# Performance work log

Hardware: AMD Instinct MI355X
Metric: run time of the kernel (lower is better)

The kernel has to match this reference:

```python
import jax, jax.numpy as jnp
import numpy as np

N, E, IN_C, HID_C, OUT_C = 50000, 800000, 64, 64, 8
NEG_SLOPE = 0.2


def setup_inputs() -> dict:
    key = jax.random.key(0)
    ks = jax.random.split(key, 12)
    return {
        "x": jax.random.normal(ks[0], (N, IN_C), dtype=jnp.float32),
        "edge_index": jax.random.randint(ks[1], (2, E), 0, N, dtype=jnp.int64),
        "edge_value": jax.random.uniform(ks[2], (E,), dtype=jnp.float32),
        "W1": jax.random.normal(ks[3], (IN_C, HID_C), dtype=jnp.float32) * 0.1,
        "a1_src": jax.random.normal(ks[4], (HID_C,), dtype=jnp.float32) * 0.1,
        "a1_dst": jax.random.normal(ks[5], (HID_C,), dtype=jnp.float32) * 0.1,
        "b1": jnp.zeros((HID_C,), dtype=jnp.float32),
        "W2": jax.random.normal(ks[6], (HID_C, OUT_C), dtype=jnp.float32) * 0.1,
        "a2_src": jax.random.normal(ks[7], (OUT_C,), dtype=jnp.float32) * 0.1,
        "a2_dst": jax.random.normal(ks[8], (OUT_C,), dtype=jnp.float32) * 0.1,
        "b2": jnp.zeros((OUT_C,), dtype=jnp.float32),
    }


def _rgat_conv(x, src, dst, edge_value, W, a_src, a_dst, b, n_nodes):
    # Linear transform: [N, out_c]
    h = x @ W
    # Per-node attention halves, gathered per edge -> per-edge logit
    e_src = h @ a_src  # [N]
    e_dst = h @ a_dst  # [N]
    logits = jax.nn.leaky_relu(e_src[src] + e_dst[dst], negative_slope=NEG_SLOPE)  # [E]
    # Segment softmax over destination neighborhoods (numerically stable)
    m = jax.ops.segment_max(logits, dst, num_segments=n_nodes)  # [N]
    ex = jnp.exp(logits - m[dst])
    denom = jax.ops.segment_sum(ex, dst, num_segments=n_nodes)  # [N]
    alpha = ex / (denom[dst] + 1e-16)  # [E]
    # Edge-weighted messages, scatter-aggregate to destinations
    msg = (alpha * edge_value)[:, None] * h[src]  # [E, out_c]
    out = jax.ops.segment_sum(msg, dst, num_segments=n_nodes)  # [N, out_c]
    return out + b


def reference(x, edge_index, edge_value, W1, a1_src, a1_dst, b1, W2, a2_src, a2_dst, b2):
    src, dst = edge_index[0], edge_index[1]
    n = x.shape[0]
    hid = _rgat_conv(x, src, dst, edge_value, W1, a1_src, a1_dst, b1, n)
    hid = jax.nn.relu(hid)
    out = _rgat_conv(hid, src, dst, edge_value, W2, a2_src, a2_dst, b2, n)
    return jax.nn.log_softmax(out, axis=1)
```

## Files before the change

### kernel.cpp

```cpp
#include <hip/hip_runtime.h>
#include <hip/hip_fp16.h>
#include <math.h>


#define CHUNK 4096
#define NBKT  256
#define CAP   6144
#define NPW   4

typedef unsigned long long ull;
typedef float v2f __attribute__((ext_vector_type(2)));

struct PartSmem {
    int lhist[NBKT], lbase[NBKT], lcur[NBKT], gbase[NBKT];
    ull buf[CHUNK];
};
struct GemmSmem {
    float4 Wl[64 * 16];
    float  Xt[64 * 64];
};
union FusedSmem { PartSmem p; GemmSmem g; };


__global__ void __launch_bounds__(256) part_gemm_kernel(
    const int* __restrict__ src, const int* __restrict__ dst,
    const float* __restrict__ ev, int* __restrict__ bcnt,
    ull* __restrict__ ped, int E, int nchunks,
    const float* __restrict__ x, const float* __restrict__ W,
    const float* __restrict__ a_src, const float* __restrict__ a_dst,
    unsigned* __restrict__ h, float* __restrict__ es, float* __restrict__ ed,
    int N)
{
    __shared__ FusedSmem sm;
    const int t = threadIdx.x;

    if (blockIdx.x < nchunks) {
        int e0 = blockIdx.x * CHUNK;
        int cnt = min(CHUNK, E - e0);
        sm.p.lhist[t] = 0;
        __syncthreads();
        for (int i = t; i < cnt; i += 256)
            atomicAdd(&sm.p.lhist[dst[e0 + i] >> 8], 1);
        __syncthreads();
        int myc = sm.p.lhist[t];
        sm.p.lbase[t] = myc;
        __syncthreads();
        for (int o = 1; o < 256; o <<= 1) {
            int add = (t >= o) ? sm.p.lbase[t - o] : 0;
            __syncthreads();
            sm.p.lbase[t] += add;
            __syncthreads();
        }
        int excl = sm.p.lbase[t] - myc;
        sm.p.gbase[t] = myc ? atomicAdd(&bcnt[t], myc) : 0;
        __syncthreads();
        sm.p.lbase[t] = excl;
        sm.p.lcur[t] = excl;
        __syncthreads();
        for (int i = t; i < cnt; i += 256) {
            int e = e0 + i;
            int d = dst[e];
            int b = d >> 8;
            unsigned p = (unsigned)src[e] | ((unsigned)(d & 255) << 16)
                       | ((unsigned)b << 24);
            ull q = (ull)p | ((ull)__float_as_uint(ev[e]) << 32);
            int r = atomicAdd(&sm.p.lcur[b], 1);
            sm.p.buf[r] = q;
        }
        __syncthreads();
        for (int i = t; i < cnt; i += 256) {
            ull q = sm.p.buf[i];
            int b = (int)((q >> 24) & 255);
            ped[(size_t)b * CAP + sm.p.gbase[b] + i - sm.p.lbase[b]] = q;
        }
        return;
    }

    const int n0 = (blockIdx.x - nchunks) * 64;

    #pragma unroll
    for (int i = 0; i < 4; ++i)
        sm.g.Wl[t + i * 256] = ((const float4*)W)[t + i * 256];

    #pragma unroll
    for (int i = 0; i < 4; ++i) {
        int f   = t + i * 256;
        int row = f >> 4, kq = f & 15;
        int grow = n0 + row;
        float4 v = make_float4(0.f, 0.f, 0.f, 0.f);
        if (grow < N) v = ((const float4*)x)[(size_t)grow * 16 + kq];
        int rs = row ^ ((kq & 3) << 2);
        sm.g.Xt[(kq * 4 + 0) * 64 + rs] = v.x;
        sm.g.Xt[(kq * 4 + 1) * 64 + rs] = v.y;
        sm.g.Xt[(kq * 4 + 2) * 64 + rs] = v.z;
        sm.g.Xt[(kq * 4 + 3) * 64 + rs] = v.w;
    }

    const int tx = t & 15;
    const int ty = t >> 4;
    const float4 asv = ((const float4*)a_src)[tx];
    const float4 adv = ((const float4*)a_dst)[tx];
    __syncthreads();

    float4 acc0 = make_float4(0.f,0.f,0.f,0.f);
    float4 acc1 = make_float4(0.f,0.f,0.f,0.f);
    float4 acc2 = make_float4(0.f,0.f,0.f,0.f);
    float4 acc3 = make_float4(0.f,0.f,0.f,0.f);

    #pragma unroll 8
    for (int k = 0; k < 64; ++k) {
        int swz = (k >> 2) & 3;
        const float4 xr = *(const float4*)&sm.g.Xt[k * 64 + ((ty ^ swz) << 2)];
        const float4 wv = sm.g.Wl[k * 16 + tx];
        acc0.x += xr.x * wv.x; acc0.y += xr.x * wv.y;
        acc0.z += xr.x * wv.z; acc0.w += xr.x * wv.w;
        acc1.x += xr.y * wv.x; acc1.y += xr.y * wv.y;
        acc1.z += xr.y * wv.z; acc1.w += xr.y * wv.w;
        acc2.x += xr.z * wv.x; acc2.y += xr.z * wv.y;
        acc2.z += xr.z * wv.z; acc2.w += xr.z * wv.w;
        acc3.x += xr.w * wv.x; acc3.y += xr.w * wv.y;
        acc3.z += xr.w * wv.z; acc3.w += xr.w * wv.w;
    }

    float4 accs[4] = {acc0, acc1, acc2, acc3};
    #pragma unroll
    for (int r = 0; r < 4; ++r) {
        int grow = n0 + ty * 4 + r;
        float4 a = accs[r];
        if (grow < N) {
            int lo = __builtin_amdgcn_cvt_pk_fp8_f32(a.x, a.y, 0, false);
            int pk = __builtin_amdgcn_cvt_pk_fp8_f32(a.z, a.w, lo, true);
            h[(size_t)grow * 16 + tx] = (unsigned)pk;
        }
        float ps = a.x * asv.x + a.y * asv.y + a.z * asv.z + a.w * asv.w;
        float pd = a.x * adv.x + a.y * adv.y + a.z * adv.z + a.w * adv.w;
        #pragma unroll
        for (int o = 8; o > 0; o >>= 1) {
            ps += __shfl_xor(ps, o);
            pd += __shfl_xor(pd, o);
        }
        if (tx == 0 && grow < N) { es[grow] = ps; ed[grow] = pd; }
    }
}


__global__ void __launch_bounds__(1024) csr2_kernel(
    const ull* __restrict__ ped, const int* __restrict__ bcnt,
    int* __restrict__ off, int* __restrict__ deg,
    ull* __restrict__ csre, int N)
{
    __shared__ int cl[256], sc[256], cur[256];
    int b = blockIdx.x, t = threadIdx.x;
    const int cnt = min(bcnt[b], CAP);
    const size_t base = (size_t)b * CAP;
    if (t < 256) cl[t] = 0;
    __syncthreads();
    for (int i = t; i < cnt; i += 1024)
        atomicAdd(&cl[(int)((ped[base + i] >> 16) & 255)], 1);
    __syncthreads();
    int myc = (t < 256) ? cl[t] : 0;
    if (t < 256) sc[t] = myc;
    __syncthreads();
    for (int o = 1; o < 256; o <<= 1) {
        int add = (t >= o && t < 256) ? sc[t - o] : 0;
        __syncthreads();
        if (t < 256) sc[t] += add;
        __syncthreads();
    }
    if (t < 256) {
        int excl = sc[t] - myc;
        int node = b * 256 + t;
        if (node < N) { off[node] = (int)base + excl; deg[node] = myc; }
        cur[t] = excl;
    }
    __syncthreads();
    for (int i = t; i < cnt; i += 1024) {
        ull q = ped[base + i];
        int dloc = (int)((q >> 16) & 255);
        int pos = (int)base + atomicAdd(&cur[dloc], 1);
        csre[pos] = (q & 0xFFFFFFFF00000000ull) | (q & 0xFFFFull);
    }
}


__global__ void __launch_bounds__(256) agg64_fused_kernel(
    const int* __restrict__ off, const int* __restrict__ deg,
    const ull* __restrict__ csre,
    const float* __restrict__ es, const float* __restrict__ ed,
    const unsigned* __restrict__ h, const float* __restrict__ b1,
    const float* __restrict__ W2, const float* __restrict__ a2s,
    const float* __restrict__ a2d, float* __restrict__ h2,
    float* __restrict__ es2, float* __restrict__ ed2, int N)
{
    const int wid = threadIdx.x >> 6, lane = threadIdx.x & 63;
    const int g  = lane >> 4;
    const int c4 = lane & 15;
    const int n0 = (blockIdx.x * 4 + wid) * NPW;
    if (n0 >= N) return;
    const int n1 = min(n0 + NPW, N);

    const int c0 = 2 * g, c1 = 2 * g + 1;
    float w2r0[4], w2r1[4];
    #pragma unroll
    for (int j = 0; j < 4; ++j) {
        w2r0[j] = W2[(4 * c4 + j) * 8 + c0];
        w2r1[j] = W2[(4 * c4 + j) * 8 + c1];
    }
    const float4 b1v = *(const float4*)&b1[c4 << 2];
    const float a2sv0 = a2s[c0], a2sv1 = a2s[c1];
    const float a2dv0 = a2d[c0], a2dv1 = a2d[c1];

    int offv = 0, degv = 0;
    float edv = 0.f;
    {
        int nn = n0 + (lane & (NPW - 1));
        if (nn < N) { offv = off[nn]; degv = deg[nn]; edv = ed[nn]; }
    }

    int svS; float evS, esS;
    unsigned pu0, pu1, pu2, pu3;
    {
        int begX = __shfl(offv, 0);
        int cntX = min(__shfl(degv, 0), 64);
        int idxX = begX + min(lane, max(cntX, 1) - 1);
        ull recX = csre[idxX];
        svS = (int)(recX & 0xFFFFull);
        evS = __uint_as_float((unsigned)(recX >> 32));
        esS = es[svS];
        int s0 = __shfl(svS, g),     s1 = __shfl(svS, 4 + g);
        int s2 = __shfl(svS, 8 + g), s3 = __shfl(svS, 12 + g);
        pu0 = h[(size_t)s0 * 16 + c4];
        pu1 = h[(size_t)s1 * 16 + c4];
        pu2 = h[(size_t)s2 * 16 + c4];
        pu3 = h[(size_t)s3 * 16 + c4];
    }

    for (int n = n0; n < n1; ++n) {
        const int nl = n - n0;
        const int beg = __shfl(offv, nl);
        const int dg  = __shfl(degv, nl);
        const float edn = __shfl(edv, nl);
        const int cnt0 = min(dg, 64);

        const int   sv = svS;
        float z = esS + edn;
        float l = z > 0.f ? z : 0.2f * z;
        float q = (lane < cnt0) ? __expf(l) : 0.f;
        float den = q;
        const float wv = q * evS;

        const unsigned cu0 = pu0, cu1 = pu1, cu2 = pu2, cu3 = pu3;

        if (n + 1 < n1) {
            int begX = __shfl(offv, nl + 1);
            int cntX = min(__shfl(degv, nl + 1), 64);
            int idxX = begX + min(lane, max(cntX, 1) - 1);
            ull recX = csre[idxX];
            svS = (int)(recX & 0xFFFFull);
            evS = __uint_as_float((unsigned)(recX >> 32));
            esS = es[svS];
            int s0 = __shfl(svS, g),     s1 = __shfl(svS, 4 + g);
            int s2 = __shfl(svS, 8 + g), s3 = __shfl(svS, 12 + g);
            pu0 = h[(size_t)s0 * 16 + c4];
            pu1 = h[(size_t)s1 * 16 + c4];
            pu2 = h[(size_t)s2 * 16 + c4];
            pu3 = h[(size_t)s3 * 16 + c4];
        }

        float4 acc = make_float4(0.f, 0.f, 0.f, 0.f);
        {
            float w0 = __shfl(wv, g),     w1 = __shfl(wv, 4 + g);
            float w2 = __shfl(wv, 8 + g), w3 = __shfl(wv, 12 + g);
            v2f f0a = __builtin_amdgcn_cvt_pk_f32_fp8((int)cu0, false);
            v2f f0b = __builtin_amdgcn_cvt_pk_f32_fp8((int)cu0, true);
            v2f f1a = __builtin_amdgcn_cvt_pk_f32_fp8((int)cu1, false);
            v2f f1b = __builtin_amdgcn_cvt_pk_f32_fp8((int)cu1, true);
            v2f f2a = __builtin_amdgcn_cvt_pk_f32_fp8((int)cu2, false);
            v2f f2b = __builtin_amdgcn_cvt_pk_f32_fp8((int)cu2, true);
            v2f f3a = __builtin_amdgcn_cvt_pk_f32_fp8((int)cu3, false);
            v2f f3b = __builtin_amdgcn_cvt_pk_f32_fp8((int)cu3, true);
            acc.x += w0 * f0a.x + w1 * f1a.x + w2 * f2a.x + w3 * f3a.x;
            acc.y += w0 * f0a.y + w1 * f1a.y + w2 * f2a.y + w3 * f3a.y;
            acc.z += w0 * f0b.x + w1 * f1b.x + w2 * f2b.x + w3 * f3b.x;
            acc.w += w0 * f0b.y + w1 * f1b.y + w2 * f2b.y + w3 * f3b.y;
        }
        for (int j = 16; j < cnt0; j += 16) {
            int j0 = j + g, j1 = j + 4 + g, j2 = j + 8 + g, j3 = j + 12 + g;
            int   s0 = __shfl(sv, j0), s1 = __shfl(sv, j1);
            int   s2 = __shfl(sv, j2), s3 = __shfl(sv, j3);
            float w0 = __shfl(wv, j0), w1 = __shfl(wv, j1);
            float w2 = __shfl(wv, j2), w3 = __shfl(wv, j3);
            const unsigned u0 = h[(size_t)s0 * 16 + c4];
            const unsigned u1 = h[(size_t)s1 * 16 + c4];
            const unsigned u2 = h[(size_t)s2 * 16 + c4];
            const unsigned u3 = h[(size_t)s3 * 16 + c4];
            v2f f0a = __builtin_amdgcn_cvt_pk_f32_fp8((int)u0, false);
            v2f f0b = __builtin_amdgcn_cvt_pk_f32_fp8((int)u0, true);
            v2f f1a = __builtin_amdgcn_cvt_pk_f32_fp8((int)u1, false);
            v2f f1b = __builtin_amdgcn_cvt_pk_f32_fp8((int)u1, true);
            v2f f2a = __builtin_amdgcn_cvt_pk_f32_fp8((int)u2, false);
            v2f f2b = __builtin_amdgcn_cvt_pk_f32_fp8((int)u2, true);
            v2f f3a = __builtin_amdgcn_cvt_pk_f32_fp8((int)u3, false);
            v2f f3b = __builtin_amdgcn_cvt_pk_f32_fp8((int)u3, true);
            acc.x += w0 * f0a.x + w1 * f1a.x + w2 * f2a.x + w3 * f3a.x;
            acc.y += w0 * f0a.y + w1 * f1a.y + w2 * f2a.y + w3 * f3a.y;
            acc.z += w0 * f0b.x + w1 * f1b.x + w2 * f2b.x + w3 * f3b.x;
            acc.w += w0 * f0b.y + w1 * f1b.y + w2 * f2b.y + w3 * f3b.y;
        }
        for (int base = beg + 64; base < beg + dg; base += 64) {
            const int cnt = min(beg + dg - base, 64);
            const int idx = base + min(lane, cnt - 1);
            const ull rec = csre[idx];
            const int sv2 = (int)(rec & 0xFFFFull);
            const float ev2 = __uint_as_float((unsigned)(rec >> 32));
            float z2 = es[sv2] + edn;
            float l2 = z2 > 0.f ? z2 : 0.2f * z2;
            float q2 = (lane < cnt) ? __expf(l2) : 0.f;
            den += q2;
            const float wv2 = q2 * ev2;
            for (int j = 0; j < cnt; j += 16) {
                int j0 = j + g, j1 = j + 4 + g, j2 = j + 8 + g, j3 = j + 12 + g;
                int   s0 = __shfl(sv2, j0), s1 = __shfl(sv2, j1);
                int   s2 = __shfl(sv2, j2), s3 = __shfl(sv2, j3);
                float w0 = __shfl(wv2, j0), w1 = __shfl(wv2, j1);
                float w2 = __shfl(wv2, j2), w3 = __shfl(wv2, j3);
                const unsigned u0 = h[(size_t)s0 * 16 + c4];
                const unsigned u1 = h[(size_t)s1 * 16 + c4];
                const unsigned u2 = h[(size_t)s2 * 16 + c4];
                const unsigned u3 = h[(size_t)s3 * 16 + c4];
                v2f f0a = __builtin_amdgcn_cvt_pk_f32_fp8((int)u0, false);
                v2f f0b = __builtin_amdgcn_cvt_pk_f32_fp8((int)u0, true);
                v2f f1a = __builtin_amdgcn_cvt_pk_f32_fp8((int)u1, false);
                v2f f1b = __builtin_amdgcn_cvt_pk_f32_fp8((int)u1, true);
                v2f f2a = __builtin_amdgcn_cvt_pk_f32_fp8((int)u2, false);
                v2f f2b = __builtin_amdgcn_cvt_pk_f32_fp8((int)u2, true);
                v2f f3a = __builtin_amdgcn_cvt_pk_f32_fp8((int)u3, false);
                v2f f3b = __builtin_amdgcn_cvt_pk_f32_fp8((int)u3, true);
                acc.x += w0 * f0a.x + w1 * f1a.x + w2 * f2a.x + w3 * f3a.x;
                acc.y += w0 * f0a.y + w1 * f1a.y + w2 * f2a.y + w3 * f3a.y;
                acc.z += w0 * f0b.x + w1 * f1b.x + w2 * f2b.x + w3 * f3b.x;
                acc.w += w0 * f0b.y + w1 * f1b.y + w2 * f2b.y + w3 * f3b.y;
            }
        }

        #pragma unroll
        for (int o = 16; o < 64; o <<= 1) {
            acc.x += __shfl_xor(acc.x, o);
            acc.y += __shfl_xor(acc.y, o);
            acc.z += __shfl_xor(acc.z, o);
            acc.w += __shfl_xor(acc.w, o);
        }
        #pragma unroll
        for (int o = 1; o < 64; o <<= 1) den += __shfl_xor(den, o);

        const float inv = 1.f / (den + 1e-16f);
        float4 hid;
        hid.x = fmaxf(acc.x * inv + b1v.x, 0.f);
        hid.y = fmaxf(acc.y * inv + b1v.y, 0.f);
        hid.z = fmaxf(acc.z * inv + b1v.z, 0.f);
        hid.w = fmaxf(acc.w * inv + b1v.w, 0.f);

        float p0 = hid.x * w2r0[0] + hid.y * w2r0[1] + hid.z * w2r0[2] + hid.w * w2r0[3];
        float p1 = hid.x * w2r1[0] + hid.y * w2r1[1] + hid.z * w2r1[2] + hid.w * w2r1[3];
        #pragma unroll
        for (int o = 1; o < 16; o <<= 1) {
            p0 += __shfl_xor(p0, o);
            p1 += __shfl_xor(p1, o);
        }
        float psv = p0 * a2sv0 + p1 * a2sv1;
        float pdv = p0 * a2dv0 + p1 * a2dv1;
        #pragma unroll
        for (int o = 16; o < 64; o <<= 1) {
            psv += __shfl_xor(psv, o);
            pdv += __shfl_xor(pdv, o);
        }
        if (c4 == 0)
            *(float2*)&h2[(size_t)n * 8 + c0] = make_float2(p0, p1);
        if (lane == 0) { es2[n] = psv; ed2[n] = pdv; }
    }
}


__global__ void __launch_bounds__(256) agg8_lsm_kernel(
    const int* __restrict__ off, const int* __restrict__ deg,
    const ull* __restrict__ csre,
    const float* __restrict__ es, const float* __restrict__ ed,
    const float* __restrict__ h2, const float* __restrict__ b,
    float* __restrict__ out, int N)
{
    const int wid = threadIdx.x >> 6, lane = threadIdx.x & 63;
    const int g  = lane >> 2;
    const int cp = lane & 3;
    const int n0 = (blockIdx.x * 4 + wid) * NPW;
    if (n0 >= N) return;
    const int n1 = min(n0 + NPW, N);
    const float bc0 = b[2 * cp], bc1 = b[2 * cp + 1];

    int offv = 0, degv = 0;
    float edv = 0.f;
    {
        int nn = n0 + (lane & (NPW - 1));
        if (nn < N) { offv = off[nn]; degv = deg[nn]; edv = ed[nn]; }
    }

    int svS; float evS, esS;
    float2 pf0, pf1;
    {
        int begX = __shfl(offv, 0);
        int cntX = min(__shfl(degv, 0), 64);
        int idxX = begX + min(lane, max(cntX, 1) - 1);
        ull recX = csre[idxX];
        svS = (int)(recX & 0xFFFFull);
        evS = __uint_as_float((unsigned)(recX >> 32));
        esS = es[svS];
        int s0 = __shfl(svS, g), s1 = __shfl(svS, 16 + g);
        pf0 = *(const float2*)&h2[(size_t)s0 * 8 + 2 * cp];
        pf1 = *(const float2*)&h2[(size_t)s1 * 8 + 2 * cp];
    }

    for (int n = n0; n < n1; ++n) {
        const int nl = n - n0;
        const int beg = __shfl(offv, nl);
        const int dg  = __shfl(degv, nl);
        const float edn = __shfl(edv, nl);
        const int cnt0 = min(dg, 64);

        const int   sv = svS;
        float z = esS + edn;
        float l = z > 0.f ? z : 0.2f * z;
        float q = (lane < cnt0) ? __expf(l) : 0.f;
        float den = q;
        const float wv = q * evS;

        const float2 cf0 = pf0, cf1 = pf1;

        if (n + 1 < n1) {
            int begX = __shfl(offv, nl + 1);
            int cntX = min(__shfl(degv, nl + 1), 64);
            int idxX = begX + min(lane, max(cntX, 1) - 1);
            ull recX = csre[idxX];
            svS = (int)(recX & 0xFFFFull);
            evS = __uint_as_float((unsigned)(recX >> 32));
            esS = es[svS];
            int s0 = __shfl(svS, g), s1 = __shfl(svS, 16 + g);
            pf0 = *(const float2*)&h2[(size_t)s0 * 8 + 2 * cp];
            pf1 = *(const float2*)&h2[(size_t)s1 * 8 + 2 * cp];
        }

        float a0, a1;
        {
            float w0 = __shfl(wv, g), w1 = __shfl(wv, 16 + g);
            a0 = w0 * cf0.x + w1 * cf1.x;
            a1 = w0 * cf0.y + w1 * cf1.y;
        }
        for (int j = 32; j < cnt0; j += 32) {
            int j0 = j + g, j1 = j + 16 + g;
            int   s0 = __shfl(sv, j0), s1 = __shfl(sv, j1);
            float w0 = __shfl(wv, j0), w1 = __shfl(wv, j1);
            const float2 f0 = *(const float2*)&h2[(size_t)s0 * 8 + 2 * cp];
            const float2 f1 = *(const float2*)&h2[(size_t)s1 * 8 + 2 * cp];
            a0 += w0 * f0.x + w1 * f1.x;
            a1 += w0 * f0.y + w1 * f1.y;
        }
        for (int base = beg + 64; base < beg + dg; base += 64) {
            const int cnt = min(beg + dg - base, 64);
            const int idx = base + min(lane, cnt - 1);
            const ull rec = csre[idx];
            const int sv2 = (int)(rec & 0xFFFFull);
            const float ev2 = __uint_as_float((unsigned)(rec >> 32));
            float z2 = es[sv2] + edn;
            float l2 = z2 > 0.f ? z2 : 0.2f * z2;
            float q2 = (lane < cnt) ? __expf(l2) : 0.f;
            den += q2;
            const float wv2 = q2 * ev2;
            for (int j = 0; j < cnt; j += 32) {
                int j0 = j + g, j1 = j + 16 + g;
                int   s0 = __shfl(sv2, j0), s1 = __shfl(sv2, j1);
                float w0 = __shfl(wv2, j0), w1 = __shfl(wv2, j1);
                const float2 f0 = *(const float2*)&h2[(size_t)s0 * 8 + 2 * cp];
                const float2 f1 = *(const float2*)&h2[(size_t)s1 * 8 + 2 * cp];
                a0 += w0 * f0.x + w1 * f1.x;
                a1 += w0 * f0.y + w1 * f1.y;
            }
        }

        #pragma unroll
        for (int o = 4; o < 64; o <<= 1) {
            a0 += __shfl_xor(a0, o);
            a1 += __shfl_xor(a1, o);
        }
        #pragma unroll
        for (int o = 1; o < 64; o <<= 1) den += __shfl_xor(den, o);

        const float inv = 1.f / (den + 1e-16f);
        float v0 = a0 * inv + bc0;
        float v1 = a1 * inv + bc1;
        float vm = fmaxf(v0, v1);
        vm = fmaxf(vm, __shfl_xor(vm, 1));
        vm = fmaxf(vm, __shfl_xor(vm, 2));
        float s = __expf(v0 - vm) + __expf(v1 - vm);
        s += __shfl_xor(s, 1);
        s += __shfl_xor(s, 2);
        float lse = vm + logf(s);
        if (lane < 4)
            *(float2*)&out[(size_t)n * 8 + 2 * cp] = make_float2(v0 - lse, v1 - lse);
    }
}


extern "C" void kernel_launch(void* const* d_in, const int* in_sizes, int n_in,
                              void* d_out, int out_size, void* d_ws, size_t ws_size,
                              hipStream_t stream)
{
    const float* x   = (const float*)d_in[0];
    const int*   ei  = (const int*)d_in[1];
    const float* ev  = (const float*)d_in[2];
    const float* W1  = (const float*)d_in[3];
    const float* a1s = (const float*)d_in[4];
    const float* a1d = (const float*)d_in[5];
    const float* b1  = (const float*)d_in[6];
    const float* W2  = (const float*)d_in[7];
    const float* a2s = (const float*)d_in[8];
    const float* a2d = (const float*)d_in[9];
    const float* b2  = (const float*)d_in[10];
    float* out = (float*)d_out;

    const int N = in_sizes[0] / 64;
    const int E = in_sizes[2];
    const int* srcp = ei;
    const int* dstp = ei + E;
    const int nchunks = (E + CHUNK - 1) / CHUNK;
    const int ngemm   = (N + 63) / 64;
    const int nbuck = (N + 255) / 256;
    const int nodes_per_block = 4 * NPW;

    ull*   ped  = (ull*)d_ws;
    ull*   csre = ped + (size_t)NBKT * CAP;
    int*   bcnt = (int*)(csre + (size_t)NBKT * CAP);
    int*   off  = bcnt + NBKT;
    int*   deg  = off + N;
    float* es1  = (float*)(deg + N);
    float* ed1  = es1 + N;
    float* es2  = ed1 + N;
    float* ed2  = es2 + N;
    unsigned* h1 = (unsigned*)(ed2 + N);
    float* h2   = (float*)(h1 + (size_t)N * 16);

    hipMemsetAsync(bcnt, 0, NBKT * sizeof(int), stream);

    part_gemm_kernel<<<nchunks + ngemm, 256, 0, stream>>>(
        srcp, dstp, ev, bcnt, ped, E, nchunks,
        x, W1, a1s, a1d, h1, es1, ed1, N);

    csr2_kernel<<<nbuck, 1024, 0, stream>>>(ped, bcnt, off, deg, csre, N);

    agg64_fused_kernel<<<(N + nodes_per_block - 1) / nodes_per_block, 256, 0, stream>>>(
        off, deg, csre, es1, ed1, h1, b1, W2, a2s, a2d, h2, es2, ed2, N);

    agg8_lsm_kernel<<<(N + nodes_per_block - 1) / nodes_per_block, 256, 0, stream>>>(
        off, deg, csre, es2, ed2, h2, b2, out, N);
}
```

Measured before the change: 158.2 us.

## Precompute layer-1 attention weights and denominators during CSR build

Moves the layer-1 edge logit, exp, edge-value product and softmax denominator into the CSR construction kernel. Per-destination sums are accumulated with shared-memory atomics, and each CSR record now stores the final weight, so the layer-1 aggregation kernel no longer gathers es or computes exp or a wavefront reduction. Because the stored weight replaces the raw edge value, the CSR kernel also writes separate source-index and edge-value arrays for a new layer-2 kernel. That adds extra global writes and workspace, and the old agg8 kernel is left as a stub full of casts to void.

Measured after the change: 167.5 us. 1.06x slower.

```diff
diff --git a/kernel.cpp b/kernel.cpp
--- a/kernel.cpp
+++ b/kernel.cpp
@@ -146,14 +146,21 @@
 
 __global__ void __launch_bounds__(1024) csr2_kernel(
     const ull* __restrict__ ped, const int* __restrict__ bcnt,
-    int* __restrict__ off, int* __restrict__ deg,
+    const float* __restrict__ es1, const float* __restrict__ ed1,
+    int* __restrict__ off, int* __restrict__ deg, float* __restrict__ den1,
     ull* __restrict__ csre, int N)
 {
     __shared__ int cl[256], sc[256], cur[256];
+    __shared__ float edl[256], denl[256];
     int b = blockIdx.x, t = threadIdx.x;
     const int cnt = min(bcnt[b], CAP);
     const size_t base = (size_t)b * CAP;
-    if (t < 256) cl[t] = 0;
+    if (t < 256) {
+        cl[t] = 0;
+        denl[t] = 0.f;
+        int node = b * 256 + t;
+        edl[t] = (node < N) ? ed1[node] : 0.f;
+    }
     __syncthreads();
     for (int i = t; i < cnt; i += 1024)
         atomicAdd(&cl[(int)((ped[base + i] >> 16) & 255)], 1);
@@ -175,18 +182,29 @@
     }
     __syncthreads();
     for (int i = t; i < cnt; i += 1024) {
-        ull q = ped[base + i];
-        int dloc = (int)((q >> 16) & 255);
+        ull qr = ped[base + i];
+        int s    = (int)(qr & 0xFFFFull);
+        int dloc = (int)((qr >> 16) & 255);
+        float evv = __uint_as_float((unsigned)(qr >> 32));
+        float z = es1[s] + edl[dloc];
+        float l = z > 0.f ? z : 0.2f * z;
+        float q = __expf(l);
+        atomicAdd(&denl[dloc], q);
+        float w = q * evv;
         int pos = (int)base + atomicAdd(&cur[dloc], 1);
-        csre[pos] = (q & 0xFFFFFFFF00000000ull) | (q & 0xFFFFull);
+        csre[pos] = ((ull)__float_as_uint(w) << 32) | (ull)(unsigned)s;
+    }
+    __syncthreads();
+    if (t < 256) {
+        int node = b * 256 + t;
+        if (node < N) den1[node] = denl[t];
     }
 }
 
 
 __global__ void __launch_bounds__(256) agg64_fused_kernel(
     const int* __restrict__ off, const int* __restrict__ deg,
-    const ull* __restrict__ csre,
-    const float* __restrict__ es, const float* __restrict__ ed,
+    const float* __restrict__ den1, const ull* __restrict__ csre,
     const unsigned* __restrict__ h, const float* __restrict__ b1,
     const float* __restrict__ W2, const float* __restrict__ a2s,
     const float* __restrict__ a2d, float* __restrict__ h2,
@@ -211,13 +229,13 @@
     const float a2dv0 = a2d[c0], a2dv1 = a2d[c1];
 
     int offv = 0, degv = 0;
-    float edv = 0.f;
+    float dnv = 0.f;
     {
         int nn = n0 + (lane & (NPW - 1));
-        if (nn < N) { offv = off[nn]; degv = deg[nn]; edv = ed[nn]; }
-    }
-
-    int svS; float evS, esS;
+        if (nn < N) { offv = off[nn]; degv = deg[nn]; dnv = den1[nn]; }
+    }
+
+    int svS; float wvS;
     unsigned pu0, pu1, pu2, pu3;
     {
         int begX = __shfl(offv, 0);
@@ -225,8 +243,7 @@
         int idxX = begX + min(lane, max(cntX, 1) - 1);
         ull recX = csre[idxX];
         svS = (int)(recX & 0xFFFFull);
-        evS = __uint_as_float((unsigned)(recX >> 32));
-        esS = es[svS];
+        wvS = __uint_as_float((unsigned)(recX >> 32));
         int s0 = __shfl(svS, g),     s1 = __shfl(svS, 4 + g);
         int s2 = __shfl(svS, 8 + g), s3 = __shfl(svS, 12 + g);
         pu0 = h[(size_t)s0 * 16 + c4];
@@ -239,15 +256,11 @@
         const int nl = n - n0;
         const int beg = __shfl(offv, nl);
         const int dg  = __shfl(degv, nl);
-        const float edn = __shfl(edv, nl);
+        float den = __shfl(dnv, nl);
         const int cnt0 = min(dg, 64);
 
         const int   sv = svS;
-        float z = esS + edn;
-        float l = z > 0.f ? z : 0.2f * z;
-        float q = (lane < cnt0) ? __expf(l) : 0.f;
-        float den = q;
-        const float wv = q * evS;
+        const float wv = (lane < cnt0) ? wvS : 0.f;
 
         const unsigned cu0 = pu0, cu1 = pu1, cu2 = pu2, cu3 = pu3;
 
@@ -257,8 +270,7 @@
             int idxX = begX + min(lane, max(cntX, 1) - 1);
             ull recX = csre[idxX];
             svS = (int)(recX & 0xFFFFull);
-            evS = __uint_as_float((unsigned)(recX >> 32));
-            esS = es[svS];
+            wvS = __uint_as_float((unsigned)(recX >> 32));
             int s0 = __shfl(svS, g),     s1 = __shfl(svS, 4 + g);
             int s2 = __shfl(svS, 8 + g), s3 = __shfl(svS, 12 + g);
             pu0 = h[(size_t)s0 * 16 + c4];
@@ -312,12 +324,7 @@
             const int idx = base + min(lane, cnt - 1);
             const ull rec = csre[idx];
             const int sv2 = (int)(rec & 0xFFFFull);
-            const float ev2 = __uint_as_float((unsigned)(rec >> 32));
-            float z2 = es[sv2] + edn;
-            float l2 = z2 > 0.f ? z2 : 0.2f * z2;
-            float q2 = (lane < cnt) ? __expf(l2) : 0.f;
-            den += q2;
-            const float wv2 = q2 * ev2;
+            const float wv2 = (lane < cnt) ? __uint_as_float((unsigned)(rec >> 32)) : 0.f;
             for (int j = 0; j < cnt; j += 16) {
                 int j0 = j + g, j1 = j + 4 + g, j2 = j + 8 + g, j3 = j + 12 + g;
                 int   s0 = __shfl(sv2, j0), s1 = __shfl(sv2, j1);
@@ -350,8 +357,6 @@
             acc.z += __shfl_xor(acc.z, o);
             acc.w += __shfl_xor(acc.w, o);
         }
-        #pragma unroll
-        for (int o = 1; o < 64; o <<= 1) den += __shfl_xor(den, o);
 
         const float inv = 1.f / (den + 1e-16f);
         float4 hid;
@@ -417,6 +422,48 @@
         pf0 = *(const float2*)&h2[(size_t)s0 * 8 + 2 * cp];
         pf1 = *(const float2*)&h2[(size_t)s1 * 8 + 2 * cp];
     }
+    (void)evS;
+
+    for (int n = n0; n < n1; ++n) (void)n;
+    (void)edv; (void)bc0; (void)bc1; (void)pf0; (void)pf1; (void)esS;
+    (void)out; (void)n1;
+}
+
+__global__ void __launch_bounds__(256) agg8_lsm2_kernel(
+    const int* __restrict__ off, const int* __restrict__ deg,
+    const int* __restrict__ csrs, const float* __restrict__ csrev,
+    const float* __restrict__ es, const float* __restrict__ ed,
+    const float* __restrict__ h2, const float* __restrict__ b,
+    float* __restrict__ out, int N)
+{
+    const int wid = threadIdx.x >> 6, lane = threadIdx.x & 63;
+    const int g  = lane >> 2;
+    const int cp = lane & 3;
+    const int n0 = (blockIdx.x * 4 + wid) * NPW;
+    if (n0 >= N) return;
+    const int n1 = min(n0 + NPW, N);
+    const float bc0 = b[2 * cp], bc1 = b[2 * cp + 1];
+
+    int offv = 0, degv = 0;
+    float edv = 0.f;
+    {
+        int nn = n0 + (lane & (NPW - 1));
+        if (nn < N) { offv = off[nn]; degv = deg[nn]; edv = ed[nn]; }
+    }
+
+    int svS; float evS, esS;
+    float2 pf0, pf1;
+    {
+        int begX = __shfl(offv, 0);
+        int cntX = min(__shfl(degv, 0), 64);
+        int idxX = begX + min(lane, max(cntX, 1) - 1);
+        svS = csrs[idxX];
+        evS = csrev[idxX];
+        esS = es[svS];
+        int s0 = __shfl(svS, g), s1 = __shfl(svS, 16 + g);
+        pf0 = *(const float2*)&h2[(size_t)s0 * 8 + 2 * cp];
+        pf1 = *(const float2*)&h2[(size_t)s1 * 8 + 2 * cp];
+    }
 
     for (int n = n0; n < n1; ++n) {
         const int nl = n - n0;
@@ -425,7 +472,7 @@
         const float edn = __shfl(edv, nl);
         const int cnt0 = min(dg, 64);
 
-        const int   sv = svS;
+        const int sv = svS;
         float z = esS + edn;
         float l = z > 0.f ? z : 0.2f * z;
         float q = (lane < cnt0) ? __expf(l) : 0.f;
@@ -438,9 +485,8 @@
             int begX = __shfl(offv, nl + 1);
             int cntX = min(__shfl(degv, nl + 1), 64);
             int idxX = begX + min(lane, max(cntX, 1) - 1);
-            ull recX = csre[idxX];
-            svS = (int)(recX & 0xFFFFull);
-            evS = __uint_as_float((unsigned)(recX >> 32));
+            svS = csrs[idxX];
+            evS = csrev[idxX];
             esS = es[svS];
             int s0 = __shfl(svS, g), s1 = __shfl(svS, 16 + g);
             pf0 = *(const float2*)&h2[(size_t)s0 * 8 + 2 * cp];
@@ -465,9 +511,8 @@
         for (int base = beg + 64; base < beg + dg; base += 64) {
             const int cnt = min(beg + dg - base, 64);
             const int idx = base + min(lane, cnt - 1);
-            const ull rec = csre[idx];
-            const int sv2 = (int)(rec & 0xFFFFull);
-            const float ev2 = __uint_as_float((unsigned)(rec >> 32));
+            const int sv2 = csrs[idx];
+            const float ev2 = csrev[idx];
             float z2 = es[sv2] + edn;
             float l2 = z2 > 0.f ? z2 : 0.2f * z2;
             float q2 = (lane < cnt) ? __expf(l2) : 0.f;
@@ -504,6 +549,66 @@
         float lse = vm + logf(s);
         if (lane < 4)
             *(float2*)&out[(size_t)n * 8 + 2 * cp] = make_float2(v0 - lse, v1 - lse);
+    }
+}
+
+__global__ void __launch_bounds__(1024) csr3_kernel(
+    const ull* __restrict__ ped, const int* __restrict__ bcnt,
+    const float* __restrict__ es1, const float* __restrict__ ed1,
+    int* __restrict__ off, int* __restrict__ deg, float* __restrict__ den1,
+    ull* __restrict__ csre, int* __restrict__ csrs, float* __restrict__ csrev,
+    int N)
+{
+    __shared__ int cl[256], sc[256], cur[256];
+    __shared__ float edl[256], denl[256];
+    int b = blockIdx.x, t = threadIdx.x;
+    const int cnt = min(bcnt[b], CAP);
+    const size_t base = (size_t)b * CAP;
+    if (t < 256) {
+        cl[t] = 0;
+        denl[t] = 0.f;
+        int node = b * 256 + t;
+        edl[t] = (node < N) ? ed1[node] : 0.f;
+    }
+    __syncthreads();
+    for (int i = t; i < cnt; i += 1024)
+        atomicAdd(&cl[(int)((ped[base + i] >> 16) & 255)], 1);
+    __syncthreads();
+    int myc = (t < 256) ? cl[t] : 0;
+    if (t < 256) sc[t] = myc;
+    __syncthreads();
+    for (int o = 1; o < 256; o <<= 1) {
+        int add = (t >= o && t < 256) ? sc[t - o] : 0;
+        __syncthreads();
+        if (t < 256) sc[t] += add;
+        __syncthreads();
+    }
+    if (t < 256) {
+        int excl = sc[t] - myc;
+        int node = b * 256 + t;
+        if (node < N) { off[node] = (int)base + excl; deg[node] = myc; }
+        cur[t] = excl;
+    }
+    __syncthreads();
+    for (int i = t; i < cnt; i += 1024) {
+        ull qr = ped[base + i];
+        int s    = (int)(qr & 0xFFFFull);
+        int dloc = (int)((qr >> 16) & 255);
+        float evv = __uint_as_float((unsigned)(qr >> 32));
+        float z = es1[s] + edl[dloc];
+        float l = z > 0.f ? z : 0.2f * z;
+        float q = __expf(l);
+        atomicAdd(&denl[dloc], q);
+        float w = q * evv;
+        int pos = (int)base + atomicAdd(&cur[dloc], 1);
+        csre[pos] = ((ull)__float_as_uint(w) << 32) | (ull)(unsigned)s;
+        csrs[pos] = s;
+        csrev[pos] = evv;
+    }
+    __syncthreads();
+    if (t < 256) {
+        int node = b * 256 + t;
+        if (node < N) den1[node] = denl[t];
     }
 }
 
@@ -534,17 +639,20 @@
     const int nbuck = (N + 255) / 256;
     const int nodes_per_block = 4 * NPW;
 
-    ull*   ped  = (ull*)d_ws;
-    ull*   csre = ped + (size_t)NBKT * CAP;
-    int*   bcnt = (int*)(csre + (size_t)NBKT * CAP);
-    int*   off  = bcnt + NBKT;
-    int*   deg  = off + N;
-    float* es1  = (float*)(deg + N);
-    float* ed1  = es1 + N;
-    float* es2  = ed1 + N;
-    float* ed2  = es2 + N;
+    ull*   ped   = (ull*)d_ws;
+    ull*   csre  = ped + (size_t)NBKT * CAP;
+    int*   csrs  = (int*)(csre + (size_t)NBKT * CAP);
+    float* csrev = (float*)(csrs + (size_t)NBKT * CAP);
+    int*   bcnt  = (int*)(csrev + (size_t)NBKT * CAP);
+    int*   off   = bcnt + NBKT;
+    int*   deg   = off + N;
+    float* den1  = (float*)(deg + N);
+    float* es1   = den1 + N;
+    float* ed1   = es1 + N;
+    float* es2   = ed1 + N;
+    float* ed2   = es2 + N;
     unsigned* h1 = (unsigned*)(ed2 + N);
-    float* h2   = (float*)(h1 + (size_t)N * 16);
+    float* h2    = (float*)(h1 + (size_t)N * 16);
 
     hipMemsetAsync(bcnt, 0, NBKT * sizeof(int), stream);
 
@@ -552,11 +660,12 @@
         srcp, dstp, ev, bcnt, ped, E, nchunks,
         x, W1, a1s, a1d, h1, es1, ed1, N);
 
-    csr2_kernel<<<nbuck, 1024, 0, stream>>>(ped, bcnt, off, deg, csre, N);
+    csr3_kernel<<<nbuck, 1024, 0, stream>>>(
+        ped, bcnt, es1, ed1, off, deg, den1, csre, csrs, csrev, N);
 
     agg64_fused_kernel<<<(N + nodes_per_block - 1) / nodes_per_block, 256, 0, stream>>>(
-        off, deg, csre, es1, ed1, h1, b1, W2, a2s, a2d, h2, es2, ed2, N);
-
-    agg8_lsm_kernel<<<(N + nodes_per_block - 1) / nodes_per_block, 256, 0, stream>>>(
-        off, deg, csre, es2, ed2, h2, b2, out, N);
+        off, deg, den1, csre, h1, b1, W2, a2s, a2d, h2, es2, ed2, N);
+
+    agg8_lsm2_kernel<<<(N + nodes_per_block - 1) / nodes_per_block, 256, 0, stream>>>(
+        off, deg, csrs, csrev, es2, ed2, h2, b2, out, N);
 }
```

## Precompute layer-1 attention weights and softmax denominators during CSR build

Applied to the files above, without the earlier changes.

The CSR construction kernel now computes the layer-1 edge logit, its exponential, and the weighted value for each edge. It accumulates per-destination softmax denominators in shared memory and stores the weight in the CSR record, with the edge value packed as fp16 for layer 2. The layer-1 aggregation kernel then skips the es gather, the exp, and the cross-lane denominator reduction. The trade-offs are extra gather and atomic work in the CSR kernel, the loss of the segment-max subtraction, and reduced edge-value precision in layer 2.

Result: no change. 159.9 us (+1.1%).

```diff
diff --git a/kernel.cpp b/kernel.cpp
--- a/kernel.cpp
+++ b/kernel.cpp
@@ -10,6 +10,11 @@
 
 typedef unsigned long long ull;
 typedef float v2f __attribute__((ext_vector_type(2)));
+
+__device__ __forceinline__ float h16tof(unsigned bits) {
+    __half hv = *(__half*)&bits;
+    return __half2float(hv);
+}
 
 struct PartSmem {
     int lhist[NBKT], lbase[NBKT], lcur[NBKT], gbase[NBKT];
@@ -144,16 +149,23 @@
 }
 
 
-__global__ void __launch_bounds__(1024) csr2_kernel(
+__global__ void __launch_bounds__(1024) csrw_kernel(
     const ull* __restrict__ ped, const int* __restrict__ bcnt,
-    int* __restrict__ off, int* __restrict__ deg,
+    const float* __restrict__ es1, const float* __restrict__ ed1,
+    int* __restrict__ off, int* __restrict__ deg, float* __restrict__ den1,
     ull* __restrict__ csre, int N)
 {
     __shared__ int cl[256], sc[256], cur[256];
+    __shared__ float edl[256], denl[256];
     int b = blockIdx.x, t = threadIdx.x;
     const int cnt = min(bcnt[b], CAP);
     const size_t base = (size_t)b * CAP;
-    if (t < 256) cl[t] = 0;
+    if (t < 256) {
+        cl[t] = 0;
+        denl[t] = 0.f;
+        int node = b * 256 + t;
+        edl[t] = (node < N) ? ed1[node] : 0.f;
+    }
     __syncthreads();
     for (int i = t; i < cnt; i += 1024)
         atomicAdd(&cl[(int)((ped[base + i] >> 16) & 255)], 1);
@@ -175,18 +187,32 @@
     }
     __syncthreads();
     for (int i = t; i < cnt; i += 1024) {
-        ull q = ped[base + i];
-        int dloc = (int)((q >> 16) & 255);
+        ull qr = ped[base + i];
+        int s    = (int)(qr & 0xFFFFull);
+        int dloc = (int)((qr >> 16) & 255);
+        float evv = __uint_as_float((unsigned)(qr >> 32));
+        float z = es1[s] + edl[dloc];
+        float l = z > 0.f ? z : 0.2f * z;
+        float q = __expf(l);
+        atomicAdd(&denl[dloc], q);
+        float w = q * evv;
+        __half evh = __float2half(evv);
+        unsigned evb = (unsigned)*(unsigned short*)&evh;
         int pos = (int)base + atomicAdd(&cur[dloc], 1);
-        csre[pos] = (q & 0xFFFFFFFF00000000ull) | (q & 0xFFFFull);
+        csre[pos] = ((ull)__float_as_uint(w) << 32) | ((ull)evb << 16)
+                  | (ull)(unsigned)s;
+    }
+    __syncthreads();
+    if (t < 256) {
+        int node = b * 256 + t;
+        if (node < N) den1[node] = denl[t];
     }
 }
 
 
 __global__ void __launch_bounds__(256) agg64_fused_kernel(
     const int* __restrict__ off, const int* __restrict__ deg,
-    const ull* __restrict__ csre,
-    const float* __restrict__ es, const float* __restrict__ ed,
+    const float* __restrict__ den1, const ull* __restrict__ csre,
     const unsigned* __restrict__ h, const float* __restrict__ b1,
     const float* __restrict__ W2, const float* __restrict__ a2s,
     const float* __restrict__ a2d, float* __restrict__ h2,
@@ -211,13 +237,13 @@
     const float a2dv0 = a2d[c0], a2dv1 = a2d[c1];
 
     int offv = 0, degv = 0;
-    float edv = 0.f;
+    float dnv = 0.f;
     {
         int nn = n0 + (lane & (NPW - 1));
-        if (nn < N) { offv = off[nn]; degv = deg[nn]; edv = ed[nn]; }
-    }
-
-    int svS; float evS, esS;
+        if (nn < N) { offv = off[nn]; degv = deg[nn]; dnv = den1[nn]; }
+    }
+
+    int svS; float wvS;
     unsigned pu0, pu1, pu2, pu3;
     {
         int begX = __shfl(offv, 0);
@@ -225,8 +251,7 @@
         int idxX = begX + min(lane, max(cntX, 1) - 1);
         ull recX = csre[idxX];
         svS = (int)(recX & 0xFFFFull);
-        evS = __uint_as_float((unsigned)(recX >> 32));
-        esS = es[svS];
+        wvS = __uint_as_float((unsigned)(recX >> 32));
         int s0 = __shfl(svS, g),     s1 = __shfl(svS, 4 + g);
         int s2 = __shfl(svS, 8 + g), s3 = __shfl(svS, 12 + g);
         pu0 = h[(size_t)s0 * 16 + c4];
@@ -239,15 +264,11 @@
         const int nl = n - n0;
         const int beg = __shfl(offv, nl);
         const int dg  = __shfl(degv, nl);
-        const float edn = __shfl(edv, nl);
+        float den = __shfl(dnv, nl);
         const int cnt0 = min(dg, 64);
 
         const int   sv = svS;
-        float z = esS + edn;
-        float l = z > 0.f ? z : 0.2f * z;
-        float q = (lane < cnt0) ? __expf(l) : 0.f;
-        float den = q;
-        const float wv = q * evS;
+        const float wv = (lane < cnt0) ? wvS : 0.f;
 
         const unsigned cu0 = pu0, cu1 = pu1, cu2 = pu2, cu3 = pu3;
 
@@ -257,8 +278,7 @@
             int idxX = begX + min(lane, max(cntX, 1) - 1);
             ull recX = csre[idxX];
             svS = (int)(recX & 0xFFFFull);
-            evS = __uint_as_float((unsigned)(recX >> 32));
-            esS = es[svS];
+            wvS = __uint_as_float((unsigned)(recX >> 32));
             int s0 = __shfl(svS, g),     s1 = __shfl(svS, 4 + g);
             int s2 = __shfl(svS, 8 + g), s3 = __shfl(svS, 12 + g);
             pu0 = h[(size_t)s0 * 16 + c4];
@@ -312,12 +332,7 @@
             const int idx = base + min(lane, cnt - 1);
             const ull rec = csre[idx];
             const int sv2 = (int)(rec & 0xFFFFull);
-            const float ev2 = __uint_as_float((unsigned)(rec >> 32));
-            float z2 = es[sv2] + edn;
-            float l2 = z2 > 0.f ? z2 : 0.2f * z2;
-            float q2 = (lane < cnt) ? __expf(l2) : 0.f;
-            den += q2;
-            const float wv2 = q2 * ev2;
+            const float wv2 = (lane < cnt) ? __uint_as_float((unsigned)(rec >> 32)) : 0.f;
             for (int j = 0; j < cnt; j += 16) {
                 int j0 = j + g, j1 = j + 4 + g, j2 = j + 8 + g, j3 = j + 12 + g;
                 int   s0 = __shfl(sv2, j0), s1 = __shfl(sv2, j1);
@@ -350,8 +365,6 @@
             acc.z += __shfl_xor(acc.z, o);
             acc.w += __shfl_xor(acc.w, o);
         }
-        #pragma unroll
-        for (int o = 1; o < 64; o <<= 1) den += __shfl_xor(den, o);
 
         const float inv = 1.f / (den + 1e-16f);
         float4 hid;
@@ -411,7 +424,7 @@
         int idxX = begX + min(lane, max(cntX, 1) - 1);
         ull recX = csre[idxX];
         svS = (int)(recX & 0xFFFFull);
-        evS = __uint_as_float((unsigned)(recX >> 32));
+        evS = h16tof((unsigned)((recX >> 16) & 0xFFFFull));
         esS = es[svS];
         int s0 = __shfl(svS, g), s1 = __shfl(svS, 16 + g);
         pf0 = *(const float2*)&h2[(size_t)s0 * 8 + 2 * cp];
@@ -425,7 +438,7 @@
         const float edn = __shfl(edv, nl);
         const int cnt0 = min(dg, 64);
 
-        const int   sv = svS;
+        const int sv = svS;
         float z = esS + edn;
         float l = z > 0.f ? z : 0.2f * z;
         float q = (lane < cnt0) ? __expf(l) : 0.f;
@@ -440,7 +453,7 @@
             int idxX = begX + min(lane, max(cntX, 1) - 1);
             ull recX = csre[idxX];
             svS = (int)(recX & 0xFFFFull);
-            evS = __uint_as_float((unsigned)(recX >> 32));
+            evS = h16tof((unsigned)((recX >> 16) & 0xFFFFull));
             esS = es[svS];
             int s0 = __shfl(svS, g), s1 = __shfl(svS, 16 + g);
             pf0 = *(const float2*)&h2[(size_t)s0 * 8 + 2 * cp];
@@ -467,7 +480,7 @@
             const int idx = base + min(lane, cnt - 1);
             const ull rec = csre[idx];
             const int sv2 = (int)(rec & 0xFFFFull);
-            const float ev2 = __uint_as_float((unsigned)(rec >> 32));
+            const float ev2 = h16tof((unsigned)((rec >> 16) & 0xFFFFull));
             float z2 = es[sv2] + edn;
             float l2 = z2 > 0.f ? z2 : 0.2f * z2;
             float q2 = (lane < cnt) ? __expf(l2) : 0.f;
@@ -534,17 +547,18 @@
     const int nbuck = (N + 255) / 256;
     const int nodes_per_block = 4 * NPW;
 
-    ull*   ped  = (ull*)d_ws;
-    ull*   csre = ped + (size_t)NBKT * CAP;
-    int*   bcnt = (int*)(csre + (size_t)NBKT * CAP);
-    int*   off  = bcnt + NBKT;
-    int*   deg  = off + N;
-    float* es1  = (float*)(deg + N);
-    float* ed1  = es1 + N;
-    float* es2  = ed1 + N;
-    float* ed2  = es2 + N;
+    ull*   ped   = (ull*)d_ws;
+    ull*   csre  = ped + (size_t)NBKT * CAP;
+    int*   bcnt  = (int*)(csre + (size_t)NBKT * CAP);
+    int*   off   = bcnt + NBKT;
+    int*   deg   = off + N;
+    float* den1  = (float*)(deg + N);
+    float* es1   = den1 + N;
+    float* ed1   = es1 + N;
+    float* es2   = ed1 + N;
+    float* ed2   = es2 + N;
     unsigned* h1 = (unsigned*)(ed2 + N);
-    float* h2   = (float*)(h1 + (size_t)N * 16);
+    float* h2    = (float*)(h1 + (size_t)N * 16);
 
     hipMemsetAsync(bcnt, 0, NBKT * sizeof(int), stream);
 
@@ -552,10 +566,11 @@
         srcp, dstp, ev, bcnt, ped, E, nchunks,
         x, W1, a1s, a1d, h1, es1, ed1, N);
 
-    csr2_kernel<<<nbuck, 1024, 0, stream>>>(ped, bcnt, off, deg, csre, N);
+    csrw_kernel<<<nbuck, 1024, 0, stream>>>(
+        ped, bcnt, es1, ed1, off, deg, den1, csre, N);
 
     agg64_fused_kernel<<<(N + nodes_per_block - 1) / nodes_per_block, 256, 0, stream>>>(
-        off, deg, csre, es1, ed1, h1, b1, W2, a2s, a2d, h2, es2, ed2, N);
+        off, deg, den1, csre, h1, b1, W2, a2s, a2d, h2, es2, ed2, N);
 
     agg8_lsm_kernel<<<(N + nodes_per_block - 1) / nodes_per_block, 256, 0, stream>>>(
         off, deg, csre, es2, ed2, h2, b2, out, N);
```
